# Kernel optimization log

Measured on AMD Instinct MI355X. Metric: run time of the kernel, lower is better.

## Reference

```python
import jax, jax.numpy as jnp
import numpy as np

BLOCK_K = 128  # per_1x128 block quantization: block_n=1 (per row), block_k=128


def _dequant(wq, scale):
    # wq: [E, N, K] quantized codes; scale: [E, N, ceil(K/BLOCK_K)]
    K = wq.shape[-1]
    s_full = jnp.repeat(scale, BLOCK_K, axis=-1)[..., :K]
    return wq * s_full


def setup_inputs() -> dict:
    key = jax.random.key(0)
    ks = jax.random.split(key, 6)
    T, E, H, I = 1024, 8, 1024, 768
    x = jax.random.normal(ks[0], (T, H), dtype=jnp.float32)
    router_logits = jax.random.normal(ks[1], (T, E), dtype=jnp.float32)
    # fp8 codes simulated as float values; block scales positive (scale_inv)
    w13_weight = jax.random.normal(ks[2], (E, 2 * I, H), dtype=jnp.float32) * 0.05
    w13_weight_scale_inv = jax.random.uniform(ks[3], (E, 2 * I, H // BLOCK_K), dtype=jnp.float32, minval=0.5, maxval=1.5)
    w2_weight = jax.random.normal(ks[4], (E, H, I), dtype=jnp.float32) * 0.05
    w2_weight_scale_inv = jax.random.uniform(ks[5], (E, H, I // BLOCK_K), dtype=jnp.float32, minval=0.5, maxval=1.5)
    return {
        "x": x,
        "router_logits": router_logits,
        "w13_weight": w13_weight,
        "w13_weight_scale_inv": w13_weight_scale_inv,
        "w2_weight": w2_weight,
        "w2_weight_scale_inv": w2_weight_scale_inv,
        "top_k": 2,
    }


def reference(x, router_logits, w13_weight, w13_weight_scale_inv, w2_weight, w2_weight_scale_inv, top_k):
    T, H = x.shape
    E = router_logits.shape[-1]
    I = w2_weight.shape[-1]

    # ---- dequantize block-scaled weights (inline dequant of fp8 grouped GEMM) ----
    w13 = _dequant(w13_weight, w13_weight_scale_inv)   # [E, 2I, H]
    w2 = _dequant(w2_weight, w2_weight_scale_inv)      # [E, H, I]

    # ---- routing: softmax scoring, top_k, renormalize ----
    probs = jax.nn.softmax(router_logits, axis=-1)     # [T, E]
    topk_w, topk_idx = jax.lax.top_k(probs, top_k)     # [T, K]
    topk_w = topk_w / jnp.sum(topk_w, axis=-1, keepdims=True)  # renormalize=True
    # dense combine weights [T, E] (scatter of top_k routing weights)
    combine = jnp.zeros((T, E), x.dtype).at[jnp.arange(T)[:, None], topk_idx].add(topk_w)

    # ---- grouped expert FFN (dense-over-experts reference) ----
    gate_up = jnp.einsum('th,enh->ten', x, w13)        # [T, E, 2I]
    gate, up = gate_up[..., :I], gate_up[..., I:]
    act = jax.nn.silu(gate) * up                       # silu activation ('silu')
    out_e = jnp.einsum('tei,ehi->teh', act, w2)        # [T, E, H]

    # ---- combine ----
    return jnp.einsum('teh,te->th', out_e, combine)    # [T, H]
```

## Files before the change

kernel.cpp:

```cpp
#include <hip/hip_runtime.h>

#define T_TOK 1024
#define H_DIM 1024
#define I_DIM 768
#define E_NUM 8

#define G13 1572864
#define G2   786432
#define GX   131072

typedef __bf16 bf16x8 __attribute__((ext_vector_type(8)));
typedef float  f32x4  __attribute__((ext_vector_type(4)));

__device__ inline bf16x8 cvt8(float4 a, float4 b, float s) {
    bf16x8 o;
    o[0] = (__bf16)(a.x * s); o[1] = (__bf16)(a.y * s);
    o[2] = (__bf16)(a.z * s); o[3] = (__bf16)(a.w * s);
    o[4] = (__bf16)(b.x * s); o[5] = (__bf16)(b.y * s);
    o[6] = (__bf16)(b.z * s); o[7] = (__bf16)(b.w * s);
    return o;
}

__global__ __launch_bounds__(256) void prep_kernel(
    const float* __restrict__ w13, const float* __restrict__ w13s,
    const float* __restrict__ w2,  const float* __restrict__ w2s,
    const float* __restrict__ x,   float4* __restrict__ out4,
    __bf16* __restrict__ w13d, __bf16* __restrict__ w2d, __bf16* __restrict__ xbf)
{
    int g = blockIdx.x * 256 + threadIdx.x;
    if (g < G13) {
        int k8 = g & 127;
        int row = g >> 7;
        float s = w13s[(row << 3) | (k8 >> 4)];
        const float4* src = (const float4*)w13 + (size_t)g * 2;
        *(bf16x8*)(w13d + (size_t)g * 8) = cvt8(src[0], src[1], s);
    } else if (g < G13 + G2) {
        int g2 = g - G13;
        unsigned row = (unsigned)g2 / 96u;
        int k8 = g2 - row * 96;
        float s = w2s[row * 6 + (k8 >> 4)];
        const float4* src = (const float4*)w2 + (size_t)g2 * 2;
        *(bf16x8*)(w2d + (size_t)g2 * 8) = cvt8(src[0], src[1], s);
    } else if (g < G13 + G2 + GX) {
        int gx = g - (G13 + G2);
        const float4* src = (const float4*)x + (size_t)gx * 2;
        *(bf16x8*)(xbf + (size_t)gx * 8) = cvt8(src[0], src[1], 1.0f);
    } else {
        int go = g - (G13 + G2 + GX);
        float4 z = make_float4(0.f, 0.f, 0.f, 0.f);
        out4[2 * go] = z; out4[2 * go + 1] = z;
    }
}

__global__ __launch_bounds__(1024) void router_kernel(
    const float* __restrict__ logits,
    int* __restrict__ counts, int* __restrict__ base,
    int* __restrict__ tok_list, float* __restrict__ wt_list)
{
    __shared__ int cnt[E_NUM];
    const int t = threadIdx.x;
    if (t < E_NUM) cnt[t] = 0;
    __syncthreads();
    float l[E_NUM];
#pragma unroll
    for (int e = 0; e < E_NUM; e++) l[e] = logits[t * E_NUM + e];
    int e0 = 0; float m0 = l[0];
#pragma unroll
    for (int e = 1; e < E_NUM; e++) if (l[e] > m0) { m0 = l[e]; e0 = e; }
    int e1 = -1; float m1 = -3e38f;
#pragma unroll
    for (int e = 0; e < E_NUM; e++) if (e != e0 && l[e] > m1) { m1 = l[e]; e1 = e; }
    float w0 = 1.0f / (1.0f + expf(m1 - m0));
    float w1 = 1.0f - w0;
    int p0 = atomicAdd(&cnt[e0], 1);
    tok_list[e0 * T_TOK + p0] = t;
    wt_list[e0 * T_TOK + p0] = w0;
    int p1 = atomicAdd(&cnt[e1], 1);
    tok_list[e1 * T_TOK + p1] = t;
    wt_list[e1 * T_TOK + p1] = w1;
    __syncthreads();
    if (t == 0) {
        int s = 0;
        for (int e = 0; e < E_NUM; e++) { base[e] = s; counts[e] = cnt[e]; s += cnt[e]; }
    }
}

#define MFMA(A, B, C) __builtin_amdgcn_mfma_f32_16x16x32_bf16(A, B, C, 0, 0, 0)

struct Stage { uint4 a0, a1, b0, b1, b2, b3; };

__device__ inline Stage ld_stage(const __bf16* pA0, const __bf16* pA1,
                                 const __bf16* pB, int k) {
    Stage s;
    s.a0 = *(const uint4*)(pA0 + k);
    s.a1 = *(const uint4*)(pA1 + k);
    s.b0 = *(const uint4*)(pB + k);
    s.b1 = *(const uint4*)(pB + k + 8);
    s.b2 = *(const uint4*)(pB + k + 16);
    s.b3 = *(const uint4*)(pB + k + 24);
    return s;
}

__device__ inline void st_stage(char* As, char* Bs, int aw0, int aw1,
                                int bw0, int bw1, int bw2, int bw3,
                                const Stage& s) {
    *(uint4*)(As + aw0) = s.a0;
    *(uint4*)(As + aw1) = s.a1;
    *(uint4*)(Bs + bw0) = s.b0;
    *(uint4*)(Bs + bw1) = s.b1;
    *(uint4*)(Bs + bw2) = s.b2;
    *(uint4*)(Bs + bw3) = s.b3;
}

__global__ __launch_bounds__(256, 3) void gemm1_kernel(
    const __bf16* __restrict__ xbf,
    const __bf16* __restrict__ w13d,
    const int* __restrict__ counts,
    const int* __restrict__ base,
    const int* __restrict__ tok_list,
    __bf16* __restrict__ act)
{
    const int bx = blockIdx.x;
    const int xcd = bx & 7, t = bx >> 3;
    const int p = t % 12, m = t / 12;
    const int P = xcd + 8 * p;
    const int nb = P % 12, e = P / 12;
    const int count = counts[e];
    const int m0 = m * 64;
    if (m0 >= count) return;
    const int n0 = nb * 64;
    const int abase = base[e];

    __shared__ union {
        struct { __bf16 Bs[2][128 * 64]; __bf16 As[2][64 * 64]; } s;
        float gu[64 * 132];
    } u;
    __shared__ int tokS[64];

    const int tid = threadIdx.x;
    if (tid < 64) {
        int r = m0 + tid;
        tokS[tid] = (r < count) ? tok_list[e * T_TOK + r] : tok_list[e * T_TOK];
    }
    __syncthreads();

    const int arow = tid >> 3, ag = tid & 7;
    const __bf16* pA0 = xbf + (size_t)tokS[arow] * H_DIM + ag * 8;
    const __bf16* pA1 = xbf + (size_t)tokS[arow + 32] * H_DIM + ag * 8;
    const int aw0 = arow * 128 + ((ag ^ (arow & 7)) << 4);
    const int aw1 = aw0 + 32 * 128;
    const int brow = tid >> 1, bg0 = (tid & 1) * 4;
    const int nB = (brow < 64) ? (n0 + brow) : (I_DIM + n0 + brow - 64);
    const __bf16* pB = w13d + ((size_t)e * 2 * I_DIM + nB) * H_DIM + bg0 * 8;
    const int bw0 = brow * 128 + (((bg0 + 0) ^ (brow & 7)) << 4);
    const int bw1 = brow * 128 + (((bg0 + 1) ^ (brow & 7)) << 4);
    const int bw2 = brow * 128 + (((bg0 + 2) ^ (brow & 7)) << 4);
    const int bw3 = brow * 128 + (((bg0 + 3) ^ (brow & 7)) << 4);

    const int wid = tid >> 6, lane = tid & 63, lrow = lane & 15, quad = lane >> 4;
    int aoff[2][4], boff[2][2];
#pragma unroll
    for (int kk = 0; kk < 2; kk++) {
        int gph = ((kk * 4 + quad) ^ (lrow & 7)) << 4;
#pragma unroll
        for (int i = 0; i < 4; i++) aoff[kk][i] = (i * 16 + lrow) * 128 + gph;
#pragma unroll
        for (int j = 0; j < 2; j++) boff[kk][j] = (wid * 32 + j * 16 + lrow) * 128 + gph;
    }

    f32x4 acc[4][2];
#pragma unroll
    for (int i = 0; i < 4; i++)
#pragma unroll
        for (int j = 0; j < 2; j++) { f32x4 z = {0.f, 0.f, 0.f, 0.f}; acc[i][j] = z; }

    char* A0 = (char*)u.s.As[0]; char* A1 = (char*)u.s.As[1];
    char* B0 = (char*)u.s.Bs[0]; char* B1 = (char*)u.s.Bs[1];

    auto compute = [&](const char* Ab, const char* Bb) {
#pragma unroll
        for (int kk = 0; kk < 2; kk++) {
            bf16x8 b0 = *(const bf16x8*)(Bb + boff[kk][0]);
            bf16x8 b1 = *(const bf16x8*)(Bb + boff[kk][1]);
#pragma unroll
            for (int i = 0; i < 4; i++) {
                bf16x8 a = *(const bf16x8*)(Ab + aoff[kk][i]);
                acc[i][0] = MFMA(a, b0, acc[i][0]);
                acc[i][1] = MFMA(a, b1, acc[i][1]);
            }
        }
    };

    Stage X = ld_stage(pA0, pA1, pB, 0);
    Stage Y = ld_stage(pA0, pA1, pB, 64);
    st_stage(A0, B0, aw0, aw1, bw0, bw1, bw2, bw3, X);
    X = ld_stage(pA0, pA1, pB, 2 * 64);
    __syncthreads();

#pragma unroll
    for (int uu = 0; uu < 8; ++uu) {
        st_stage(A1, B1, aw0, aw1, bw0, bw1, bw2, bw3, Y);
        if (2 * uu + 3 < 16) Y = ld_stage(pA0, pA1, pB, (2 * uu + 3) * 64);
        compute(A0, B0);
        __syncthreads();
        if (uu < 7) st_stage(A0, B0, aw0, aw1, bw0, bw1, bw2, bw3, X);
        if (2 * uu + 4 < 16) X = ld_stage(pA0, pA1, pB, (2 * uu + 4) * 64);
        compute(A1, B1);
        __syncthreads();
    }

#pragma unroll
    for (int i = 0; i < 4; i++)
#pragma unroll
        for (int j = 0; j < 2; j++)
#pragma unroll
            for (int r = 0; r < 4; r++) {
                int mr = i * 16 + quad * 4 + r;
                int c = wid * 32 + j * 16 + lrow;
                u.gu[mr * 132 + c] = acc[i][j][r];
            }
    __syncthreads();

#pragma unroll
    for (int ii = 0; ii < 16; ii++) {
        int o = ii * 256 + tid;
        int mr = o >> 6, c = o & 63;
        if (m0 + mr < count) {
            float g  = u.gu[mr * 132 + c];
            float up = u.gu[mr * 132 + 64 + c];
            float a  = g / (1.0f + expf(-g)) * up;
            act[(size_t)(abase + m0 + mr) * I_DIM + n0 + c] = (__bf16)a;
        }
    }
}

__global__ __launch_bounds__(256, 3) void gemm2_kernel(
    const __bf16* __restrict__ act,
    const __bf16* __restrict__ w2d,
    const int* __restrict__ counts,
    const int* __restrict__ base,
    const int* __restrict__ tok_list,
    const float* __restrict__ wt_list,
    float* __restrict__ out)
{
    const int bx = blockIdx.x;
    const int xcd = bx & 7, t = bx >> 3;
    const int p = t & 7, m = t >> 3;
    const int P = xcd + 8 * p;
    const int nb = P & 7, e = P >> 3;
    const int count = counts[e];
    const int m0 = m * 64;
    if (m0 >= count) return;
    const int n0 = nb * 128;
    const int abase = base[e];

    __shared__ struct { __bf16 Bs[2][128 * 64]; __bf16 As[2][64 * 64]; } s;

    const int tid = threadIdx.x;
    const int arow = tid >> 3, ag = tid & 7;
    int gr0 = abase + m0 + arow;      if (gr0 > 2 * T_TOK - 1) gr0 = 2 * T_TOK - 1;
    int gr1 = abase + m0 + arow + 32; if (gr1 > 2 * T_TOK - 1) gr1 = 2 * T_TOK - 1;
    const __bf16* pA0 = act + (size_t)gr0 * I_DIM + ag * 8;
    const __bf16* pA1 = act + (size_t)gr1 * I_DIM + ag * 8;
    const int aw0 = arow * 128 + ((ag ^ (arow & 7)) << 4);
    const int aw1 = aw0 + 32 * 128;

    const int brow = tid >> 1, bg0 = (tid & 1) * 4;
    const __bf16* pB = w2d + ((size_t)e * H_DIM + n0 + brow) * I_DIM + bg0 * 8;
    const int bw0 = brow * 128 + (((bg0 + 0) ^ (brow & 7)) << 4);
    const int bw1 = brow * 128 + (((bg0 + 1) ^ (brow & 7)) << 4);
    const int bw2 = brow * 128 + (((bg0 + 2) ^ (brow & 7)) << 4);
    const int bw3 = brow * 128 + (((bg0 + 3) ^ (brow & 7)) << 4);

    const int wid = tid >> 6, lane = tid & 63, lrow = lane & 15, quad = lane >> 4;
    int aoff[2][4], boff[2][2];
#pragma unroll
    for (int kk = 0; kk < 2; kk++) {
        int gph = ((kk * 4 + quad) ^ (lrow & 7)) << 4;
#pragma unroll
        for (int i = 0; i < 4; i++) aoff[kk][i] = (i * 16 + lrow) * 128 + gph;
#pragma unroll
        for (int j = 0; j < 2; j++) boff[kk][j] = (wid * 32 + j * 16 + lrow) * 128 + gph;
    }

    f32x4 acc[4][2];
#pragma unroll
    for (int i = 0; i < 4; i++)
#pragma unroll
        for (int j = 0; j < 2; j++) { f32x4 z = {0.f, 0.f, 0.f, 0.f}; acc[i][j] = z; }

    char* A0 = (char*)s.As[0]; char* A1 = (char*)s.As[1];
    char* B0 = (char*)s.Bs[0]; char* B1 = (char*)s.Bs[1];

    auto compute = [&](const char* Ab, const char* Bb) {
#pragma unroll
        for (int kk = 0; kk < 2; kk++) {
            bf16x8 b0 = *(const bf16x8*)(Bb + boff[kk][0]);
            bf16x8 b1 = *(const bf16x8*)(Bb + boff[kk][1]);
#pragma unroll
            for (int i = 0; i < 4; i++) {
                bf16x8 a = *(const bf16x8*)(Ab + aoff[kk][i]);
                acc[i][0] = MFMA(a, b0, acc[i][0]);
                acc[i][1] = MFMA(a, b1, acc[i][1]);
            }
        }
    };

    Stage X = ld_stage(pA0, pA1, pB, 0);
    Stage Y = ld_stage(pA0, pA1, pB, 64);
    st_stage(A0, B0, aw0, aw1, bw0, bw1, bw2, bw3, X);
    X = ld_stage(pA0, pA1, pB, 2 * 64);
    __syncthreads();

#pragma unroll
    for (int uu = 0; uu < 6; ++uu) {
        st_stage(A1, B1, aw0, aw1, bw0, bw1, bw2, bw3, Y);
        if (2 * uu + 3 < 12) Y = ld_stage(pA0, pA1, pB, (2 * uu + 3) * 64);
        compute(A0, B0);
        __syncthreads();
        if (uu < 5) st_stage(A0, B0, aw0, aw1, bw0, bw1, bw2, bw3, X);
        if (2 * uu + 4 < 12) X = ld_stage(pA0, pA1, pB, (2 * uu + 4) * 64);
        compute(A1, B1);
        __syncthreads();
    }

#pragma unroll
    for (int i = 0; i < 4; i++)
#pragma unroll
        for (int r = 0; r < 4; r++) {
            int mr = i * 16 + quad * 4 + r;
            if (m0 + mr < count) {
                int   tk = tok_list[e * T_TOK + m0 + mr];
                float w  = wt_list[e * T_TOK + m0 + mr];
#pragma unroll
                for (int j = 0; j < 2; j++) {
                    int h = n0 + wid * 32 + j * 16 + lrow;
                    atomicAdd(&out[(size_t)tk * H_DIM + h], w * acc[i][j][r]);
                }
            }
        }
}

extern "C" void kernel_launch(void* const* d_in, const int* in_sizes, int n_in,
                              void* d_out, int out_size, void* d_ws, size_t ws_size,
                              hipStream_t stream) {
    (void)in_sizes; (void)n_in; (void)out_size; (void)ws_size;
    const float* x      = (const float*)d_in[0];
    const float* logits = (const float*)d_in[1];
    const float* w13    = (const float*)d_in[2];
    const float* w13s   = (const float*)d_in[3];
    const float* w2     = (const float*)d_in[4];
    const float* w2s    = (const float*)d_in[5];
    float* out = (float*)d_out;

    char* ws = (char*)d_ws;
    int*    counts   = (int*)ws;
    int*    base     = (int*)(ws + 128);
    int*    tok_list = (int*)(ws + 256);
    float*  wt_list  = (float*)(ws + 256 + 32768);
    __bf16* act      = (__bf16*)(ws + 65792);
    __bf16* xbf      = (__bf16*)(ws + 65792 + 3145728);
    __bf16* w13d     = (__bf16*)(ws + 65792 + 3145728 + 2097152);
    __bf16* w2d      = (__bf16*)(ws + 65792 + 3145728 + 2097152 + 25165824);

    prep_kernel<<<dim3(10240), 256, 0, stream>>>(w13, w13s, w2, w2s, x,
                                                 (float4*)out, w13d, w2d, xbf);
    router_kernel<<<dim3(1), 1024, 0, stream>>>(logits, counts, base, tok_list, wt_list);
    gemm1_kernel<<<dim3(1536), 256, 0, stream>>>(
        xbf, w13d, counts, base, tok_list, act);
    gemm2_kernel<<<dim3(1024), 256, 0, stream>>>(
        act, w2d, counts, base, tok_list, wt_list, out);
}
```

Before: 154.1 us.

## Fuse router into prep kernel, split-K gemm2, prefetch weights before token sync

The router moves into an extra block of the prep kernel, which drops one launch and lets routing run alongside the dequant work; each prep thread now handles two groups. gemm1 issues its first weight tile loads before the barrier that waits for token indices, so part of the load latency overlaps the index fetch. gemm2 is split along K into two halves, doubling the grid to 2048 blocks, and both halves atomically accumulate into the output. This raises parallelism in gemm2 at the price of twice as many atomic adds to the output.

After: 157.3 us. 2.1% more time.

```diff
diff --git a/kernel.cpp b/kernel.cpp
--- a/kernel.cpp
+++ b/kernel.cpp
@@ -8,6 +8,8 @@
 #define G13 1572864
 #define G2   786432
 #define GX   131072
+#define GTOT 2621440
+#define GHALF 1310720
 
 typedef __bf16 bf16x8 __attribute__((ext_vector_type(8)));
 typedef float  f32x4  __attribute__((ext_vector_type(4)));
@@ -21,13 +23,13 @@
     return o;
 }
 
-__global__ __launch_bounds__(256) void prep_kernel(
+__device__ inline void prep_group(
+    int g,
     const float* __restrict__ w13, const float* __restrict__ w13s,
     const float* __restrict__ w2,  const float* __restrict__ w2s,
     const float* __restrict__ x,   float4* __restrict__ out4,
     __bf16* __restrict__ w13d, __bf16* __restrict__ w2d, __bf16* __restrict__ xbf)
 {
-    int g = blockIdx.x * 256 + threadIdx.x;
     if (g < G13) {
         int k8 = g & 127;
         int row = g >> 7;
@@ -52,34 +54,48 @@
     }
 }
 
-__global__ __launch_bounds__(1024) void router_kernel(
+__global__ __launch_bounds__(256) void prep_kernel(
+    const float* __restrict__ w13, const float* __restrict__ w13s,
+    const float* __restrict__ w2,  const float* __restrict__ w2s,
+    const float* __restrict__ x,   float4* __restrict__ out4,
+    __bf16* __restrict__ w13d, __bf16* __restrict__ w2d, __bf16* __restrict__ xbf,
     const float* __restrict__ logits,
     int* __restrict__ counts, int* __restrict__ base,
     int* __restrict__ tok_list, float* __restrict__ wt_list)
 {
+    const int bx = blockIdx.x, tid = threadIdx.x;
+    if (bx < 5120) {
+        int g0 = bx * 256 + tid;
+        prep_group(g0, w13, w13s, w2, w2s, x, out4, w13d, w2d, xbf);
+        prep_group(g0 + GHALF, w13, w13s, w2, w2s, x, out4, w13d, w2d, xbf);
+        return;
+    }
     __shared__ int cnt[E_NUM];
-    const int t = threadIdx.x;
-    if (t < E_NUM) cnt[t] = 0;
-    __syncthreads();
-    float l[E_NUM];
-#pragma unroll
-    for (int e = 0; e < E_NUM; e++) l[e] = logits[t * E_NUM + e];
-    int e0 = 0; float m0 = l[0];
-#pragma unroll
-    for (int e = 1; e < E_NUM; e++) if (l[e] > m0) { m0 = l[e]; e0 = e; }
-    int e1 = -1; float m1 = -3e38f;
-#pragma unroll
-    for (int e = 0; e < E_NUM; e++) if (e != e0 && l[e] > m1) { m1 = l[e]; e1 = e; }
-    float w0 = 1.0f / (1.0f + expf(m1 - m0));
-    float w1 = 1.0f - w0;
-    int p0 = atomicAdd(&cnt[e0], 1);
-    tok_list[e0 * T_TOK + p0] = t;
-    wt_list[e0 * T_TOK + p0] = w0;
-    int p1 = atomicAdd(&cnt[e1], 1);
-    tok_list[e1 * T_TOK + p1] = t;
-    wt_list[e1 * T_TOK + p1] = w1;
-    __syncthreads();
-    if (t == 0) {
+    if (tid < E_NUM) cnt[tid] = 0;
+    __syncthreads();
+#pragma unroll
+    for (int tt = 0; tt < 4; tt++) {
+        int t = tid + tt * 256;
+        float l[E_NUM];
+#pragma unroll
+        for (int e = 0; e < E_NUM; e++) l[e] = logits[t * E_NUM + e];
+        int e0 = 0; float m0 = l[0];
+#pragma unroll
+        for (int e = 1; e < E_NUM; e++) if (l[e] > m0) { m0 = l[e]; e0 = e; }
+        int e1 = -1; float m1 = -3e38f;
+#pragma unroll
+        for (int e = 0; e < E_NUM; e++) if (e != e0 && l[e] > m1) { m1 = l[e]; e1 = e; }
+        float w0 = 1.0f / (1.0f + expf(m1 - m0));
+        float w1 = 1.0f - w0;
+        int p0 = atomicAdd(&cnt[e0], 1);
+        tok_list[e0 * T_TOK + p0] = t;
+        wt_list[e0 * T_TOK + p0] = w0;
+        int p1 = atomicAdd(&cnt[e1], 1);
+        tok_list[e1 * T_TOK + p1] = t;
+        wt_list[e1 * T_TOK + p1] = w1;
+    }
+    __syncthreads();
+    if (tid == 0) {
         int s = 0;
         for (int e = 0; e < E_NUM; e++) { base[e] = s; counts[e] = cnt[e]; s += cnt[e]; }
     }
@@ -87,25 +103,28 @@
 
 #define MFMA(A, B, C) __builtin_amdgcn_mfma_f32_16x16x32_bf16(A, B, C, 0, 0, 0)
 
-struct Stage { uint4 a0, a1, b0, b1, b2, b3; };
-
-__device__ inline Stage ld_stage(const __bf16* pA0, const __bf16* pA1,
-                                 const __bf16* pB, int k) {
-    Stage s;
+struct StA { uint4 a0, a1; };
+struct StB { uint4 b0, b1, b2, b3; };
+
+__device__ inline StA ldA(const __bf16* pA0, const __bf16* pA1, int k) {
+    StA s;
     s.a0 = *(const uint4*)(pA0 + k);
     s.a1 = *(const uint4*)(pA1 + k);
+    return s;
+}
+__device__ inline StB ldB(const __bf16* pB, int k) {
+    StB s;
     s.b0 = *(const uint4*)(pB + k);
     s.b1 = *(const uint4*)(pB + k + 8);
     s.b2 = *(const uint4*)(pB + k + 16);
     s.b3 = *(const uint4*)(pB + k + 24);
     return s;
 }
-
-__device__ inline void st_stage(char* As, char* Bs, int aw0, int aw1,
-                                int bw0, int bw1, int bw2, int bw3,
-                                const Stage& s) {
+__device__ inline void stA(char* As, int aw0, int aw1, const StA& s) {
     *(uint4*)(As + aw0) = s.a0;
     *(uint4*)(As + aw1) = s.a1;
+}
+__device__ inline void stB(char* Bs, int bw0, int bw1, int bw2, int bw3, const StB& s) {
     *(uint4*)(Bs + bw0) = s.b0;
     *(uint4*)(Bs + bw1) = s.b1;
     *(uint4*)(Bs + bw2) = s.b2;
@@ -142,13 +161,7 @@
         int r = m0 + tid;
         tokS[tid] = (r < count) ? tok_list[e * T_TOK + r] : tok_list[e * T_TOK];
     }
-    __syncthreads();
-
-    const int arow = tid >> 3, ag = tid & 7;
-    const __bf16* pA0 = xbf + (size_t)tokS[arow] * H_DIM + ag * 8;
-    const __bf16* pA1 = xbf + (size_t)tokS[arow + 32] * H_DIM + ag * 8;
-    const int aw0 = arow * 128 + ((ag ^ (arow & 7)) << 4);
-    const int aw1 = aw0 + 32 * 128;
+
     const int brow = tid >> 1, bg0 = (tid & 1) * 4;
     const int nB = (brow < 64) ? (n0 + brow) : (I_DIM + n0 + brow - 64);
     const __bf16* pB = w13d + ((size_t)e * 2 * I_DIM + nB) * H_DIM + bg0 * 8;
@@ -157,6 +170,19 @@
     const int bw2 = brow * 128 + (((bg0 + 2) ^ (brow & 7)) << 4);
     const int bw3 = brow * 128 + (((bg0 + 3) ^ (brow & 7)) << 4);
 
+    StB XB = ldB(pB, 0);
+    StB YB = ldB(pB, 64);
+    __syncthreads();
+
+    const int arow = tid >> 3, ag = tid & 7;
+    const __bf16* pA0 = xbf + (size_t)tokS[arow] * H_DIM + ag * 8;
+    const __bf16* pA1 = xbf + (size_t)tokS[arow + 32] * H_DIM + ag * 8;
+    const int aw0 = arow * 128 + ((ag ^ (arow & 7)) << 4);
+    const int aw1 = aw0 + 32 * 128;
+
+    StA XA = ldA(pA0, pA1, 0);
+    StA YA = ldA(pA0, pA1, 64);
+
     const int wid = tid >> 6, lane = tid & 63, lrow = lane & 15, quad = lane >> 4;
     int aoff[2][4], boff[2][2];
 #pragma unroll
@@ -191,20 +217,18 @@
         }
     };
 
-    Stage X = ld_stage(pA0, pA1, pB, 0);
-    Stage Y = ld_stage(pA0, pA1, pB, 64);
-    st_stage(A0, B0, aw0, aw1, bw0, bw1, bw2, bw3, X);
-    X = ld_stage(pA0, pA1, pB, 2 * 64);
+    stA(A0, aw0, aw1, XA); stB(B0, bw0, bw1, bw2, bw3, XB);
+    XA = ldA(pA0, pA1, 128); XB = ldB(pB, 128);
     __syncthreads();
 
 #pragma unroll
     for (int uu = 0; uu < 8; ++uu) {
-        st_stage(A1, B1, aw0, aw1, bw0, bw1, bw2, bw3, Y);
-        if (2 * uu + 3 < 16) Y = ld_stage(pA0, pA1, pB, (2 * uu + 3) * 64);
+        stA(A1, aw0, aw1, YA); stB(B1, bw0, bw1, bw2, bw3, YB);
+        if (2 * uu + 3 < 16) { YA = ldA(pA0, pA1, (2 * uu + 3) * 64); YB = ldB(pB, (2 * uu + 3) * 64); }
         compute(A0, B0);
         __syncthreads();
-        if (uu < 7) st_stage(A0, B0, aw0, aw1, bw0, bw1, bw2, bw3, X);
-        if (2 * uu + 4 < 16) X = ld_stage(pA0, pA1, pB, (2 * uu + 4) * 64);
+        if (uu < 7) { stA(A0, aw0, aw1, XA); stB(B0, bw0, bw1, bw2, bw3, XB); }
+        if (2 * uu + 4 < 16) { XA = ldA(pA0, pA1, (2 * uu + 4) * 64); XB = ldB(pB, (2 * uu + 4) * 64); }
         compute(A1, B1);
         __syncthreads();
     }
@@ -245,7 +269,9 @@
 {
     const int bx = blockIdx.x;
     const int xcd = bx & 7, t = bx >> 3;
-    const int p = t & 7, m = t >> 3;
+    const int kh = t & 1;
+    const int t2 = t >> 1;
+    const int p = t2 & 7, m = t2 >> 3;
     const int P = xcd + 8 * p;
     const int nb = P & 7, e = P >> 3;
     const int count = counts[e];
@@ -253,6 +279,7 @@
     if (m0 >= count) return;
     const int n0 = nb * 128;
     const int abase = base[e];
+    const int kb = kh * 384;
 
     __shared__ struct { __bf16 Bs[2][128 * 64]; __bf16 As[2][64 * 64]; } s;
 
@@ -260,13 +287,13 @@
     const int arow = tid >> 3, ag = tid & 7;
     int gr0 = abase + m0 + arow;      if (gr0 > 2 * T_TOK - 1) gr0 = 2 * T_TOK - 1;
     int gr1 = abase + m0 + arow + 32; if (gr1 > 2 * T_TOK - 1) gr1 = 2 * T_TOK - 1;
-    const __bf16* pA0 = act + (size_t)gr0 * I_DIM + ag * 8;
-    const __bf16* pA1 = act + (size_t)gr1 * I_DIM + ag * 8;
+    const __bf16* pA0 = act + (size_t)gr0 * I_DIM + kb + ag * 8;
+    const __bf16* pA1 = act + (size_t)gr1 * I_DIM + kb + ag * 8;
     const int aw0 = arow * 128 + ((ag ^ (arow & 7)) << 4);
     const int aw1 = aw0 + 32 * 128;
 
     const int brow = tid >> 1, bg0 = (tid & 1) * 4;
-    const __bf16* pB = w2d + ((size_t)e * H_DIM + n0 + brow) * I_DIM + bg0 * 8;
+    const __bf16* pB = w2d + ((size_t)e * H_DIM + n0 + brow) * I_DIM + kb + bg0 * 8;
     const int bw0 = brow * 128 + (((bg0 + 0) ^ (brow & 7)) << 4);
     const int bw1 = brow * 128 + (((bg0 + 1) ^ (brow & 7)) << 4);
     const int bw2 = brow * 128 + (((bg0 + 2) ^ (brow & 7)) << 4);
@@ -306,20 +333,22 @@
         }
     };
 
-    Stage X = ld_stage(pA0, pA1, pB, 0);
-    Stage Y = ld_stage(pA0, pA1, pB, 64);
-    st_stage(A0, B0, aw0, aw1, bw0, bw1, bw2, bw3, X);
-    X = ld_stage(pA0, pA1, pB, 2 * 64);
-    __syncthreads();
-
-#pragma unroll
-    for (int uu = 0; uu < 6; ++uu) {
-        st_stage(A1, B1, aw0, aw1, bw0, bw1, bw2, bw3, Y);
-        if (2 * uu + 3 < 12) Y = ld_stage(pA0, pA1, pB, (2 * uu + 3) * 64);
+    StA XA = ldA(pA0, pA1, 0);
+    StB XB = ldB(pB, 0);
+    StA YA = ldA(pA0, pA1, 64);
+    StB YB = ldB(pB, 64);
+    stA(A0, aw0, aw1, XA); stB(B0, bw0, bw1, bw2, bw3, XB);
+    XA = ldA(pA0, pA1, 128); XB = ldB(pB, 128);
+    __syncthreads();
+
+#pragma unroll
+    for (int uu = 0; uu < 3; ++uu) {
+        stA(A1, aw0, aw1, YA); stB(B1, bw0, bw1, bw2, bw3, YB);
+        if (2 * uu + 3 < 6) { YA = ldA(pA0, pA1, (2 * uu + 3) * 64); YB = ldB(pB, (2 * uu + 3) * 64); }
         compute(A0, B0);
         __syncthreads();
-        if (uu < 5) st_stage(A0, B0, aw0, aw1, bw0, bw1, bw2, bw3, X);
-        if (2 * uu + 4 < 12) X = ld_stage(pA0, pA1, pB, (2 * uu + 4) * 64);
+        if (uu < 2) { stA(A0, aw0, aw1, XA); stB(B0, bw0, bw1, bw2, bw3, XB); }
+        if (2 * uu + 4 < 6) { XA = ldA(pA0, pA1, (2 * uu + 4) * 64); XB = ldB(pB, (2 * uu + 4) * 64); }
         compute(A1, B1);
         __syncthreads();
     }
@@ -363,11 +392,11 @@
     __bf16* w13d     = (__bf16*)(ws + 65792 + 3145728 + 2097152);
     __bf16* w2d      = (__bf16*)(ws + 65792 + 3145728 + 2097152 + 25165824);
 
-    prep_kernel<<<dim3(10240), 256, 0, stream>>>(w13, w13s, w2, w2s, x,
-                                                 (float4*)out, w13d, w2d, xbf);
-    router_kernel<<<dim3(1), 1024, 0, stream>>>(logits, counts, base, tok_list, wt_list);
+    prep_kernel<<<dim3(5121), 256, 0, stream>>>(
+        w13, w13s, w2, w2s, x, (float4*)out, w13d, w2d, xbf,
+        logits, counts, base, tok_list, wt_list);
     gemm1_kernel<<<dim3(1536), 256, 0, stream>>>(
         xbf, w13d, counts, base, tok_list, act);
-    gemm2_kernel<<<dim3(1024), 256, 0, stream>>>(
+    gemm2_kernel<<<dim3(2048), 256, 0, stream>>>(
         act, w2d, counts, base, tok_list, wt_list, out);
 }
```
